# Kernel tuning notes

Hardware: AMD Instinct MI355X
Metric: run time of the kernel (lower is better)

## Reference

```python
import jax, jax.numpy as jnp
import numpy as np

B, T, N, D = 16, 24, 2048, 64
L, K = 2, 3  # num_layers, cheb_k


def setup_inputs() -> dict:
    key = jax.random.key(0)
    ks = jax.random.split(key, 6)
    x = jax.random.normal(ks[0], (B, T, N, D), dtype=jnp.float32)
    init_state = jnp.zeros((L, B, N, D), dtype=jnp.float32)
    adj = jax.random.uniform(ks[1], (N, N), dtype=jnp.float32)
    adj = adj / jnp.sum(adj, axis=-1, keepdims=True)  # row-normalized adjacency
    cin = 2 * D
    Wg = jax.random.normal(ks[2], (L, K, cin, 2 * D), dtype=jnp.float32) * (1.0 / np.sqrt(K * cin))
    bg = jnp.zeros((L, 2 * D), dtype=jnp.float32)
    Wu = jax.random.normal(ks[3], (L, K, cin, D), dtype=jnp.float32) * (1.0 / np.sqrt(K * cin))
    bu = jnp.zeros((L, D), dtype=jnp.float32)
    return {"x": x, "init_state": init_state, "adj_matrix": adj,
            "Wg": Wg, "bg": bg, "Wu": Wu, "bu": bu}


def _cheb_supports(adj, k):
    # T0=I, T1=A, Tk = 2*A@T_{k-1} - T_{k-2}
    n = adj.shape[0]
    sup = [jnp.eye(n, dtype=adj.dtype), adj]
    for _ in range(2, k):
        sup.append(2.0 * adj @ sup[-1] - sup[-2])
    return jnp.stack(sup[:k], axis=0)  # [K, N, N]


def _gconv(xs, supports, W, b):
    # xs: [B,N,Cin], supports: [K,N,N], W: [K,Cin,Cout]
    xg = jnp.einsum('knm,bmc->bknc', supports, xs)
    return jnp.einsum('bknc,kco->bno', xg, W) + b


def _cell(x_t, state, supports, Wg_l, bg_l, Wu_l, bu_l):
    ins = jnp.concatenate([x_t, state], axis=-1)  # [B,N,2D]
    zr = jax.nn.sigmoid(_gconv(ins, supports, Wg_l, bg_l))
    z, r = jnp.split(zr, 2, axis=-1)
    cand_in = jnp.concatenate([x_t, z * state], axis=-1)
    hc = jnp.tanh(_gconv(cand_in, supports, Wu_l, bu_l))
    return r * state + (1.0 - r) * hc


def reference(x, init_state, adj_matrix, Wg, bg, Wu, bu):
    supports = _cheb_supports(adj_matrix, K)
    current = x  # [B,T,N,D]
    hiddens = []
    for l in range(L):
        def step(state, x_t, l=l):
            new = _cell(x_t, state, supports, Wg[l], bg[l], Wu[l], bu[l])
            return new, new
        last, seq = jax.lax.scan(step, init_state[l], jnp.swapaxes(current, 0, 1))
        hiddens.append(last)
        current = x + jnp.swapaxes(seq, 0, 1)  # residual over the stacked states
    return current, jnp.stack(hiddens, axis=0)
```

## Files before the change

kernel.cpp:

```cpp
#include <hip/hip_runtime.h>
#include <hip/hip_bf16.h>
#include <math.h>

typedef __bf16 bf16x8 __attribute__((ext_vector_type(8)));
typedef float f32x4 __attribute__((ext_vector_type(4)));
typedef __hip_bfloat16 bf16s;

constexpr int kB = 16, kT = 24, kN = 2048, kD = 64;
constexpr size_t kBND = (size_t)kB * kN * kD;

struct SlotDesc { const void* p; int astr; int trow; int isF32; };
struct Slots6 { SlotDesc s[6]; };
struct DiffGrp { const bf16s* src; bf16s* oA; bf16s* oA2; };
struct DiffP { const bf16s* S0; const bf16s* S1; DiffGrp g[4]; int colsPerGrp; };

__device__ __forceinline__ void async_copy16(void* lds, const void* g) {
  __builtin_amdgcn_global_load_lds((const __attribute__((address_space(1))) void*)g,
                                   (__attribute__((address_space(3))) void*)lds,
                                   16, 0, 0);
}


__device__ __forceinline__ void diff_core(
    const bf16s* __restrict__ S, const bf16s* __restrict__ Bsrc,
    int m0, int c0, bf16s* lA, bf16s* lB, f32x4 (&acc)[4][4])
{
  const int tid = threadIdx.x, lane = tid & 63, wave = tid >> 6;
  const int wm = (wave >> 1) * 64, wn = (wave & 1) * 64;
  const f32x4 zero = {0.f, 0.f, 0.f, 0.f};
#pragma unroll
  for (int i = 0; i < 4; ++i)
#pragma unroll
    for (int j = 0; j < 4; ++j) acc[i][j] = zero;

  const int ra = tid >> 3;
  const int cs = ((tid & 7) ^ (ra & 7)) * 8;
  const int rk0 = (((lane >> 4)) ^ (lane & 7)) * 8;
  const int rk1 = ((4 + (lane >> 4)) ^ (lane & 7)) * 8;

  for (int k0 = 0; k0 < 2048; k0 += 64) {
#pragma unroll
    for (int i = 0; i < 4; ++i)
      async_copy16(lA + (size_t)(i * 256 + tid) * 8,
                   S + (size_t)(m0 + i * 32 + ra) * 2048 + k0 + cs);
#pragma unroll
    for (int i = 0; i < 4; ++i)
      async_copy16(lB + (size_t)(i * 256 + tid) * 8,
                   Bsrc + (size_t)(c0 + i * 32 + ra) * 2048 + k0 + cs);
    __syncthreads();
#pragma unroll
    for (int ks = 0; ks < 2; ++ks) {
      const int rk = ks ? rk1 : rk0;
      bf16x8 av[4], bv[4];
#pragma unroll
      for (int f = 0; f < 4; ++f) {
        av[f] = *(const bf16x8*)(lA + (size_t)(wm + f * 16 + (lane & 15)) * 64 + rk);
        bv[f] = *(const bf16x8*)(lB + (size_t)(wn + f * 16 + (lane & 15)) * 64 + rk);
      }
#pragma unroll
      for (int i = 0; i < 4; ++i)
#pragma unroll
        for (int j = 0; j < 4; ++j)
          acc[i][j] = __builtin_amdgcn_mfma_f32_16x16x32_bf16(av[i], bv[j], acc[i][j], 0, 0, 0);
    }
    __syncthreads();
  }
}

__global__ __launch_bounds__(256) void k_diff(DiffP p)
{
  __shared__ bf16s lA[128 * 64];
  __shared__ bf16s lB[128 * 64];
  const int mi = blockIdx.x;
  const bf16s* S = (mi >> 4) ? p.S1 : p.S0;
  const int m0 = (mi & 15) * 128;
  const int ybpg = p.colsPerGrp >> 7;
  const int grp = blockIdx.y / ybpg;
  const int c0 = (blockIdx.y - grp * ybpg) * 128;
  const DiffGrp G = p.g[grp];

  f32x4 acc[4][4];
  diff_core(S, G.src, m0, c0, lA, lB, acc);

  bf16s* out = (mi >> 4) ? G.oA2 : G.oA;
  const int lane = threadIdx.x & 63, wave = threadIdx.x >> 6;
  const int wm = (wave >> 1) * 64, wn = (wave & 1) * 64;
  const int rq = (lane >> 4) * 4, cl = lane & 15;
#pragma unroll
  for (int fm = 0; fm < 4; ++fm)
#pragma unroll
    for (int fn = 0; fn < 4; ++fn)
#pragma unroll
      for (int q = 0; q < 4; ++q) {
        int gm = m0 + wm + fm * 16 + rq + q;
        int gc = c0 + wn + fn * 16 + cl;
        size_t off = ((size_t)(gc >> 6) * 2048 + gm) * 64 + (gc & 63);
        out[off] = __float2bfloat16(acc[fm][fn][q]);
      }
}

__global__ __launch_bounds__(256) void k_a2(
    const bf16s* __restrict__ A, const bf16s* __restrict__ AT, bf16s* A2)
{
  __shared__ bf16s lA[128 * 64];
  __shared__ bf16s lB[128 * 64];
  const int m0 = blockIdx.x * 128, n0 = blockIdx.y * 128;
  f32x4 acc[4][4];
  diff_core(A, AT, m0, n0, lA, lB, acc);
  const int lane = threadIdx.x & 63, wave = threadIdx.x >> 6;
  const int wm = (wave >> 1) * 64, wn = (wave & 1) * 64;
  const int rq = (lane >> 4) * 4, cl = lane & 15;
#pragma unroll
  for (int fm = 0; fm < 4; ++fm)
#pragma unroll
    for (int fn = 0; fn < 4; ++fn)
#pragma unroll
      for (int q = 0; q < 4; ++q) {
        int gm = m0 + wm + fm * 16 + rq + q;
        int gc = n0 + wn + fn * 16 + cl;
        A2[(size_t)gm * 2048 + gc] = __float2bfloat16(2.f * acc[fm][fn][q] - (gm == gc ? 1.f : 0.f));
      }
}

template<int BN>
__device__ __forceinline__ void small_core(
    const Slots6& sl, int m0, const bf16s* __restrict__ W,
    bf16s* lA, bf16s* lB, f32x4 (&acc)[4][BN / 32])
{
  const int tid = threadIdx.x, lane = tid & 63, wave = tid >> 6;
  const int wm = (wave >> 1) * 64, wn = (wave & 1) * (BN / 2);
  const f32x4 zero = {0.f, 0.f, 0.f, 0.f};
#pragma unroll
  for (int i = 0; i < 4; ++i)
#pragma unroll
    for (int j = 0; j < BN / 32; ++j) acc[i][j] = zero;

  const int ra = tid >> 3;
  const int cs = ((tid & 7) ^ (ra & 7)) * 8;
  const int rk0 = (((lane >> 4)) ^ (lane & 7)) * 8;
  const int rk1 = ((4 + (lane >> 4)) ^ (lane & 7)) * 8;

#pragma unroll
  for (int ks = 0; ks < 6; ++ks) {
    const SlotDesc sd = sl.s[ks];
    if (!sd.isF32) {
      const bf16s* base = (const bf16s*)sd.p;
#pragma unroll
      for (int i = 0; i < 4; ++i) {
        int row = m0 + i * 32 + ra;
        size_t roff = ((size_t)(row >> 11) * sd.astr + sd.trow + (row & 2047)) * 64 + cs;
        async_copy16(lA + (size_t)(i * 256 + tid) * 8, base + roff);
      }
    } else {
#pragma unroll
      for (int i = 0; i < 4; ++i) {
        int row = m0 + i * 32 + ra;
        size_t roff = ((size_t)(row >> 11) * sd.astr + sd.trow + (row & 2047)) * 64 + cs;
        const float4* q0 = (const float4*)((const float*)sd.p + roff);
        float4 a = q0[0], b = q0[1];
        union { bf16x8 v; bf16s h[8]; } u;
        u.h[0] = __float2bfloat16(a.x); u.h[1] = __float2bfloat16(a.y);
        u.h[2] = __float2bfloat16(a.z); u.h[3] = __float2bfloat16(a.w);
        u.h[4] = __float2bfloat16(b.x); u.h[5] = __float2bfloat16(b.y);
        u.h[6] = __float2bfloat16(b.z); u.h[7] = __float2bfloat16(b.w);
        *(bf16x8*)(lA + (size_t)(i * 256 + tid) * 8) = u.v;
      }
    }
#pragma unroll
    for (int i = 0; i < BN / 32; ++i)
      async_copy16(lB + (size_t)(i * 256 + tid) * 8,
                   W + (size_t)(i * 32 + ra) * 384 + ks * 64 + cs);
    __syncthreads();
#pragma unroll
    for (int kss = 0; kss < 2; ++kss) {
      const int rk = kss ? rk1 : rk0;
      bf16x8 av[4], bv[BN / 32];
#pragma unroll
      for (int f = 0; f < 4; ++f)
        av[f] = *(const bf16x8*)(lA + (size_t)(wm + f * 16 + (lane & 15)) * 64 + rk);
#pragma unroll
      for (int f = 0; f < BN / 32; ++f)
        bv[f] = *(const bf16x8*)(lB + (size_t)(wn + f * 16 + (lane & 15)) * 64 + rk);
#pragma unroll
      for (int i = 0; i < 4; ++i)
#pragma unroll
        for (int j = 0; j < BN / 32; ++j)
          acc[i][j] = __builtin_amdgcn_mfma_f32_16x16x32_bf16(av[i], bv[j], acc[i][j], 0, 0, 0);
    }
    __syncthreads();
  }
}

struct LayerG {
  Slots6 sl; const bf16s* W; const float* bias;
  const float* h; bf16s* zh; bf16s* zhT; float* r;
};
__global__ __launch_bounds__(256) void k_gate(LayerG A, LayerG B, int nA)
{
  __shared__ bf16s lA[128 * 64];
  __shared__ bf16s lB[128 * 64];
  const int bx = blockIdx.x;
  const bool isA = bx < nA;
  const LayerG L = isA ? A : B;
  const int m0 = (isA ? bx : bx - nA) * 128;
  f32x4 acc[4][4];
  small_core<128>(L.sl, m0, L.W, lA, lB, acc);
  const int lane = threadIdx.x & 63, wave = threadIdx.x >> 6;
  const int wm = (wave >> 1) * 64, wn = (wave & 1) * 64;
  const int rq = (lane >> 4) * 4, cl = lane & 15;
#pragma unroll
  for (int fm = 0; fm < 4; ++fm)
#pragma unroll
    for (int fn = 0; fn < 4; ++fn) {
      const int o = wn + fn * 16 + cl;
      const float bias = L.bias[o];
#pragma unroll
      for (int q = 0; q < 4; ++q) {
        size_t gm = (size_t)m0 + wm + fm * 16 + rq + q;
        float s = 1.f / (1.f + expf(-(acc[fm][fn][q] + bias)));
        if (o < 64) {
          float zh = s * L.h[gm * 64 + o];
          L.zh[gm * 64 + o] = __float2bfloat16(zh);
          L.zhT[((size_t)((gm >> 11) * 64 + o)) * 2048 + (gm & 2047)] = __float2bfloat16(zh);
        } else {
          L.r[gm * 64 + (o - 64)] = s;
        }
      }
    }
}

struct LayerC {
  Slots6 sl; const bf16s* W; const float* bias;
  const float* r; float* h32; bf16s* hT; bf16s* h_bf; float* hid;
  bf16s* x1; bf16s* x1T;
  float* outC;
  const float* x0; int t;
};
__global__ __launch_bounds__(256) void k_cand(LayerC A, LayerC B, int nA)
{
  __shared__ bf16s lA[128 * 64];
  __shared__ bf16s lB[64 * 64];
  const int bx = blockIdx.x;
  const bool isA = bx < nA;
  const LayerC L = isA ? A : B;
  const int m0 = (isA ? bx : bx - nA) * 128;
  f32x4 acc[4][2];
  small_core<64>(L.sl, m0, L.W, lA, lB, acc);
  const int lane = threadIdx.x & 63, wave = threadIdx.x >> 6;
  const int wm = (wave >> 1) * 64, wn = (wave & 1) * 32;
  const int rq = (lane >> 4) * 4, cl = lane & 15;
#pragma unroll
  for (int fm = 0; fm < 4; ++fm)
#pragma unroll
    for (int fn = 0; fn < 2; ++fn) {
      const int d = wn + fn * 16 + cl;
      const float bias = L.bias[d];
#pragma unroll
      for (int q = 0; q < 4; ++q) {
        size_t gm = (size_t)m0 + wm + fm * 16 + rq + q;
        float hc = tanhf(acc[fm][fn][q] + bias);
        float r = L.r[gm * 64 + d];
        float h = L.h32[gm * 64 + d];
        float hn = r * h + (1.f - r) * hc;
        L.h32[gm * 64 + d] = hn;
        int b = (int)(gm >> 11), n = (int)(gm & 2047);
        L.hT[((size_t)(b * 64 + d)) * 2048 + n] = __float2bfloat16(hn);
        L.h_bf[gm * 64 + d] = __float2bfloat16(hn);
        size_t xi = (((size_t)b * kT + L.t) * 2048 + n) * 64 + d;
        if (L.x1) {
          float xv = L.x0[xi] + hn;
          L.x1[gm * 64 + d] = __float2bfloat16(xv);
          L.x1T[((size_t)(b * 64 + d)) * 2048 + n] = __float2bfloat16(xv);
        }
        if (L.outC) L.outC[xi] = L.x0[xi] + hn;
        if (L.hid) L.hid[gm * 64 + d] = hn;
      }
    }
}

__global__ __launch_bounds__(256) void transpose_cvt(
    const float* in, bf16s* out, int nrows, int ncols,
    size_t in_ostride, size_t out_ostride)
{
  __shared__ float tile[64][65];
  const int r0 = blockIdx.x * 64, c0 = blockIdx.y * 64;
  in  += (size_t)blockIdx.z * in_ostride;
  out += (size_t)blockIdx.z * out_ostride;
  const int tx = threadIdx.x & 63, ty = threadIdx.x >> 6;
#pragma unroll
  for (int i = 0; i < 64; i += 4)
    tile[ty + i][tx] = in[(size_t)(r0 + ty + i) * ncols + c0 + tx];
  __syncthreads();
#pragma unroll
  for (int i = 0; i < 64; i += 4)
    out[(size_t)(c0 + ty + i) * nrows + r0 + tx] = __float2bfloat16(tile[tx][ty + i]);
}

__global__ __launch_bounds__(256) void k_cvt(const float* in, bf16s* out, int n)
{
  int i = blockIdx.x * 256 + threadIdx.x;
  if (i < n) out[i] = __float2bfloat16(in[i]);
}

__global__ __launch_bounds__(256) void k_repack(
    const float* Wg, const float* Wu, bf16s* WgT, bf16s* WuT)
{
  int idx = blockIdx.x * 256 + threadIdx.x;
  if (idx < 2 * 3 * 128 * 128) {
    int o = idx & 127, cin = (idx >> 7) & 127, k = (idx >> 14) % 3, l = idx / 49152;
    WgT[((size_t)(l * 128 + o)) * 384 + (2 * k + (cin >> 6)) * 64 + (cin & 63)] =
        __float2bfloat16(Wg[idx]);
  }
  if (idx < 2 * 3 * 128 * 64) {
    int o = idx & 63, cin = (idx >> 6) & 127, k = (idx >> 13) % 3, l = idx / 24576;
    WuT[((size_t)(l * 64 + o)) * 384 + (2 * k + (cin >> 6)) * 64 + (cin & 63)] =
        __float2bfloat16(Wu[idx]);
  }
}

__global__ __launch_bounds__(256) void init_layer(
    const float* ist_l, float* h32, bf16s* hT, bf16s* h_bf)
{
  size_t idx = (size_t)blockIdx.x * 256 + threadIdx.x;
  if (idx >= kBND) return;
  int d = (int)(idx & 63);
  size_t row = idx >> 6;
  int n = (int)(row & 2047), b = (int)(row >> 11);
  float h = ist_l[idx];
  h32[idx] = h;
  hT[((size_t)(b * 64 + d)) * 2048 + n] = __float2bfloat16(h);
  h_bf[idx] = __float2bfloat16(h);
}

extern "C" void kernel_launch(void* const* d_in, const int* in_sizes, int n_in,
                              void* d_out, int out_size, void* d_ws, size_t ws_size,
                              hipStream_t stream)
{
  (void)in_sizes; (void)n_in; (void)out_size;
  const float* x   = (const float*)d_in[0];
  const float* ist = (const float*)d_in[1];
  const float* adj = (const float*)d_in[2];
  const float* Wg  = (const float*)d_in[3];
  const float* bg  = (const float*)d_in[4];
  const float* Wu  = (const float*)d_in[5];
  const float* bu  = (const float*)d_in[6];
  float* outCur = (float*)d_out;
  float* outHid = outCur + (size_t)kB * kT * kN * kD;

  char* p = (char*)d_ws;
  auto carve = [&](size_t bytes) { char* q = p; p += (bytes + 255) & ~(size_t)255; return q; };
  bf16s* A_bf  = (bf16s*)carve((size_t)2048 * 2048 * 2);
  bf16s* A2_bf = (bf16s*)carve((size_t)2048 * 2048 * 2);
  bf16s* WgT   = (bf16s*)carve((size_t)2 * 128 * 384 * 2);
  bf16s* WuT   = (bf16s*)carve((size_t)2 * 64 * 384 * 2);
  float* h32b  = (float*)carve(2 * kBND * 4);
  float* r32b  = (float*)carve(2 * kBND * 4);
  bf16s* hTb   = (bf16s*)carve(2 * kBND * 2);
  bf16s* hbfb  = (bf16s*)carve(2 * kBND * 2);
  bf16s* zhTb  = (bf16s*)carve(2 * kBND * 2);
  bf16s* zhbfb = (bf16s*)carve(2 * kBND * 2);
  bf16s* x1_bf = (bf16s*)carve(kBND * 2);
  bf16s* x1T   = (bf16s*)carve(kBND * 2);
  bf16s* sAh0  = (bf16s*)carve(kBND * 2);
  bf16s* sA2h0 = (bf16s*)carve(kBND * 2);
  bf16s* sAh1  = (bf16s*)carve(kBND * 2);
  bf16s* sA2h1 = (bf16s*)carve(kBND * 2);
  bf16s* sAx1  = (bf16s*)carve(kBND * 2);
  bf16s* sA2x1 = (bf16s*)carve(kBND * 2);

  float* h32_0 = h32b;            float* h32_1 = h32b + kBND;
  float* r32_0 = r32b;            float* r32_1 = r32b + kBND;
  bf16s* hT0 = hTb;               bf16s* hT1 = hTb + kBND;
  bf16s* hbf0 = hbfb;             bf16s* hbf1 = hbfb + kBND;
  bf16s* zhT0 = zhTb;             bf16s* zhT1 = zhTb + kBND;
  bf16s* zhbf0 = zhbfb;           bf16s* zhbf1 = zhbfb + kBND;

  size_t used = (size_t)(p - (char*)d_ws);
  size_t rem = (ws_size > used) ? ws_size - used : 0;
  const size_t xTfull = (size_t)kB * kT * kD * kN * 2;
  bool batched0 = rem >= (xTfull / 2 + 2 * xTfull + (1 << 20));

  bf16s *AT_bf, *AxF = nullptr, *A2xF = nullptr, *xTh = nullptr;
  bf16s *x0T = nullptr, *sAx0 = nullptr, *sA2x0 = nullptr;
  if (batched0) {
    AxF  = (bf16s*)carve(xTfull);
    A2xF = (bf16s*)carve(xTfull);
    xTh  = (bf16s*)carve(xTfull / 2);
    AT_bf = AxF;
  } else {
    AT_bf = (bf16s*)carve((size_t)2048 * 2048 * 2);
    x0T   = (bf16s*)carve(kBND * 2);
    sAx0  = (bf16s*)carve(kBND * 2);
    sA2x0 = (bf16s*)carve(kBND * 2);
  }

  k_cvt<<<dim3((2048 * 2048 + 255) / 256), 256, 0, stream>>>(adj, A_bf, 2048 * 2048);
  transpose_cvt<<<dim3(32, 32, 1), 256, 0, stream>>>(adj, AT_bf, 2048, 2048, 0, 0);
  k_a2<<<dim3(16, 16, 1), 256, 0, stream>>>(A_bf, AT_bf, A2_bf);
  k_repack<<<dim3(384), 256, 0, stream>>>(Wg, Wu, WgT, WuT);
  init_layer<<<dim3((int)(kBND / 256)), 256, 0, stream>>>(ist, h32_0, hT0, hbf0);
  init_layer<<<dim3((int)(kBND / 256)), 256, 0, stream>>>(ist + kBND, h32_1, hT1, hbf1);

  if (batched0) {
    for (int h = 0; h < 2; ++h) {
      size_t off = (size_t)h * 8 * kT * 131072;
      transpose_cvt<<<dim3(32, 1, 8 * kT), 256, 0, stream>>>(x + off, xTh, 2048, 64, 131072, 131072);
      DiffP dp; dp.S0 = A_bf; dp.S1 = A2_bf; dp.colsPerGrp = 12288;
      dp.g[0] = DiffGrp{xTh, AxF + off, A2xF + off};
      dp.g[1] = dp.g[2] = dp.g[3] = DiffGrp{nullptr, nullptr, nullptr};
      k_diff<<<dim3(32, 96), 256, 0, stream>>>(dp);
    }
  }

  for (int s = 0; s <= kT; ++s) {
    const bool aA = (s < kT), aB = (s >= 1);
    const int tA = s, tB = s - 1;
    const int nA = aA ? 256 : 0, nB = aB ? 256 : 0;

    if (aA && !batched0)
      transpose_cvt<<<dim3(32, 1, kB), 256, 0, stream>>>(
          x + (size_t)tA * 131072, x0T, 2048, 64, (size_t)kT * 131072, 131072);

    {
      DiffP dp; dp.S0 = A_bf; dp.S1 = A2_bf; dp.colsPerGrp = 1024;
      int ng = 0;
      if (aA)              dp.g[ng++] = DiffGrp{hT0, sAh0, sA2h0};
      if (aA && !batched0) dp.g[ng++] = DiffGrp{x0T, sAx0, sA2x0};
      if (aB) { dp.g[ng++] = DiffGrp{hT1, sAh1, sA2h1};
                dp.g[ng++] = DiffGrp{x1T, sAx1, sA2x1}; }
      for (int i = ng; i < 4; ++i) dp.g[i] = DiffGrp{nullptr, nullptr, nullptr};
      k_diff<<<dim3(32, 8 * ng), 256, 0, stream>>>(dp);
    }

    {
      LayerG GA = {}, GB = {};
      if (aA) {
        GA.sl.s[0] = SlotDesc{x, kT * 2048, tA * 2048, 1};
        GA.sl.s[1] = SlotDesc{hbf0, 2048, 0, 0};
        GA.sl.s[2] = batched0 ? SlotDesc{AxF,  kT * 2048, tA * 2048, 0} : SlotDesc{sAx0, 2048, 0, 0};
        GA.sl.s[3] = SlotDesc{sAh0, 2048, 0, 0};
        GA.sl.s[4] = batched0 ? SlotDesc{A2xF, kT * 2048, tA * 2048, 0} : SlotDesc{sA2x0, 2048, 0, 0};
        GA.sl.s[5] = SlotDesc{sA2h0, 2048, 0, 0};
        GA.W = WgT; GA.bias = bg; GA.h = h32_0; GA.zh = zhbf0; GA.zhT = zhT0; GA.r = r32_0;
      }
      if (aB) {
        GB.sl.s[0] = SlotDesc{x1_bf, 2048, 0, 0};
        GB.sl.s[1] = SlotDesc{hbf1, 2048, 0, 0};
        GB.sl.s[2] = SlotDesc{sAx1, 2048, 0, 0};
        GB.sl.s[3] = SlotDesc{sAh1, 2048, 0, 0};
        GB.sl.s[4] = SlotDesc{sA2x1, 2048, 0, 0};
        GB.sl.s[5] = SlotDesc{sA2h1, 2048, 0, 0};
        GB.W = WgT + (size_t)128 * 384; GB.bias = bg + 128;
        GB.h = h32_1; GB.zh = zhbf1; GB.zhT = zhT1; GB.r = r32_1;
      }
      k_gate<<<dim3(nA + nB), 256, 0, stream>>>(GA, GB, nA);
    }

    {
      DiffP dp; dp.S0 = A_bf; dp.S1 = A2_bf; dp.colsPerGrp = 1024;
      int ng = 0;
      if (aA) dp.g[ng++] = DiffGrp{zhT0, sAh0, sA2h0};
      if (aB) dp.g[ng++] = DiffGrp{zhT1, sAh1, sA2h1};
      for (int i = ng; i < 4; ++i) dp.g[i] = DiffGrp{nullptr, nullptr, nullptr};
      k_diff<<<dim3(32, 8 * ng), 256, 0, stream>>>(dp);
    }

    {
      LayerC CA = {}, CB = {};
      if (aA) {
        CA.sl = LayerG{}.sl;
        CA.sl.s[0] = SlotDesc{x, kT * 2048, tA * 2048, 1};
        CA.sl.s[1] = SlotDesc{zhbf0, 2048, 0, 0};
        CA.sl.s[2] = batched0 ? SlotDesc{AxF,  kT * 2048, tA * 2048, 0} : SlotDesc{sAx0, 2048, 0, 0};
        CA.sl.s[3] = SlotDesc{sAh0, 2048, 0, 0};
        CA.sl.s[4] = batched0 ? SlotDesc{A2xF, kT * 2048, tA * 2048, 0} : SlotDesc{sA2x0, 2048, 0, 0};
        CA.sl.s[5] = SlotDesc{sA2h0, 2048, 0, 0};
        CA.W = WuT; CA.bias = bu; CA.r = r32_0; CA.h32 = h32_0; CA.hT = hT0; CA.h_bf = hbf0;
        CA.hid = (tA == kT - 1) ? outHid : nullptr;
        CA.x1 = x1_bf; CA.x1T = x1T; CA.outC = nullptr; CA.x0 = x; CA.t = tA;
      }
      if (aB) {
        CB.sl.s[0] = SlotDesc{x1_bf, 2048, 0, 0};
        CB.sl.s[1] = SlotDesc{zhbf1, 2048, 0, 0};
        CB.sl.s[2] = SlotDesc{sAx1, 2048, 0, 0};
        CB.sl.s[3] = SlotDesc{sAh1, 2048, 0, 0};
        CB.sl.s[4] = SlotDesc{sA2x1, 2048, 0, 0};
        CB.sl.s[5] = SlotDesc{sA2h1, 2048, 0, 0};
        CB.W = WuT + (size_t)64 * 384; CB.bias = bu + 64;
        CB.r = r32_1; CB.h32 = h32_1; CB.hT = hT1; CB.h_bf = hbf1;
        CB.hid = (tB == kT - 1) ? outHid + kBND : nullptr;
        CB.x1 = nullptr; CB.x1T = nullptr; CB.outC = outCur; CB.x0 = x; CB.t = tB;
      }
      k_cand<<<dim3(nA + nB), 256, 0, stream>>>(CA, CB, nA);
    }
  }
}
```

Measured before the change: 5.224 ms.

## Exploit linearity to drop layer-1 x diffusion; fuse A and A2 diffusion per block

Layer 1's input is x + h0_new, so A·x1 is rebuilt as A·x + A·h0 from the already computed per-step diffusion of layer 0's state and the batched x diffusion. This removes the x1 transpose and its per-step diffusion GEMMs, and the candidate stage adds two bf16 operands while loading. A new 512-thread diffusion kernel computes A·B and A²·B in one block, sharing the B tile in LDS across both supports. The batched x path is now always used, and the candidate diffusion outputs go to separate buffers so that sAh0 is not overwritten. The sum is formed from bf16 values, which adds a small precision risk.

```diff
diff --git a/kernel.cpp b/kernel.cpp
--- a/kernel.cpp
+++ b/kernel.cpp
@@ -9,10 +9,9 @@
 constexpr int kB = 16, kT = 24, kN = 2048, kD = 64;
 constexpr size_t kBND = (size_t)kB * kN * kD;
 
-struct SlotDesc { const void* p; int astr; int trow; int isF32; };
-struct Slots6 { SlotDesc s[6]; };
-struct DiffGrp { const bf16s* src; bf16s* oA; bf16s* oA2; };
-struct DiffP { const bf16s* S0; const bf16s* S1; DiffGrp g[4]; int colsPerGrp; };
+struct Slot { const void* p0; const void* p1; int astr0, trow0, astr1, trow1, type; };
+struct Slots6 { Slot s[6]; };
+struct DiffSrc { const bf16s* src; bf16s* oA; bf16s* oA2; };
 
 __device__ __forceinline__ void async_copy16(void* lds, const void* g) {
   __builtin_amdgcn_global_load_lds((const __attribute__((address_space(1))) void*)g,
@@ -21,12 +20,24 @@
 }
 
 
-__device__ __forceinline__ void diff_core(
-    const bf16s* __restrict__ S, const bf16s* __restrict__ Bsrc,
-    int m0, int c0, bf16s* lA, bf16s* lB, f32x4 (&acc)[4][4])
-{
+__global__ __launch_bounds__(512) void k_diff4(
+    const bf16s* __restrict__ S0, const bf16s* __restrict__ S1,
+    DiffSrc g0, DiffSrc g1, int ctPerSrc)
+{
+  __shared__ bf16s lA0[128 * 64];
+  __shared__ bf16s lA1[128 * 64];
+  __shared__ bf16s lB[128 * 64];
+  const int m0 = blockIdx.x * 128;
+  const int grp = blockIdx.y / ctPerSrc;
+  const int c0 = (blockIdx.y - grp * ctPerSrc) * 128;
+  const DiffSrc G = grp ? g1 : g0;
+
   const int tid = threadIdx.x, lane = tid & 63, wave = tid >> 6;
-  const int wm = (wave >> 1) * 64, wn = (wave & 1) * 64;
+  const int sp = wave & 1, qd = wave >> 1;
+  const int wm = (qd >> 1) * 64, wn = (qd & 1) * 64;
+  const bf16s* lAsel = sp ? lA1 : lA0;
+
+  f32x4 acc[4][4];
   const f32x4 zero = {0.f, 0.f, 0.f, 0.f};
 #pragma unroll
   for (int i = 0; i < 4; ++i)
@@ -35,18 +46,22 @@
 
   const int ra = tid >> 3;
   const int cs = ((tid & 7) ^ (ra & 7)) * 8;
-  const int rk0 = (((lane >> 4)) ^ (lane & 7)) * 8;
+  const int rk0 = ((lane >> 4) ^ (lane & 7)) * 8;
   const int rk1 = ((4 + (lane >> 4)) ^ (lane & 7)) * 8;
 
   for (int k0 = 0; k0 < 2048; k0 += 64) {
 #pragma unroll
-    for (int i = 0; i < 4; ++i)
-      async_copy16(lA + (size_t)(i * 256 + tid) * 8,
-                   S + (size_t)(m0 + i * 32 + ra) * 2048 + k0 + cs);
-#pragma unroll
-    for (int i = 0; i < 4; ++i)
-      async_copy16(lB + (size_t)(i * 256 + tid) * 8,
-                   Bsrc + (size_t)(c0 + i * 32 + ra) * 2048 + k0 + cs);
+    for (int i = 0; i < 2; ++i)
+      async_copy16(lA0 + (size_t)(i * 512 + tid) * 8,
+                   S0 + (size_t)(m0 + i * 64 + ra) * 2048 + k0 + cs);
+#pragma unroll
+    for (int i = 0; i < 2; ++i)
+      async_copy16(lA1 + (size_t)(i * 512 + tid) * 8,
+                   S1 + (size_t)(m0 + i * 64 + ra) * 2048 + k0 + cs);
+#pragma unroll
+    for (int i = 0; i < 2; ++i)
+      async_copy16(lB + (size_t)(i * 512 + tid) * 8,
+                   G.src + (size_t)(c0 + i * 64 + ra) * 2048 + k0 + cs);
     __syncthreads();
 #pragma unroll
     for (int ks = 0; ks < 2; ++ks) {
@@ -54,7 +69,7 @@
       bf16x8 av[4], bv[4];
 #pragma unroll
       for (int f = 0; f < 4; ++f) {
-        av[f] = *(const bf16x8*)(lA + (size_t)(wm + f * 16 + (lane & 15)) * 64 + rk);
+        av[f] = *(const bf16x8*)(lAsel + (size_t)(wm + f * 16 + (lane & 15)) * 64 + rk);
         bv[f] = *(const bf16x8*)(lB + (size_t)(wn + f * 16 + (lane & 15)) * 64 + rk);
       }
 #pragma unroll
@@ -65,26 +80,8 @@
     }
     __syncthreads();
   }
-}
-
-__global__ __launch_bounds__(256) void k_diff(DiffP p)
-{
-  __shared__ bf16s lA[128 * 64];
-  __shared__ bf16s lB[128 * 64];
-  const int mi = blockIdx.x;
-  const bf16s* S = (mi >> 4) ? p.S1 : p.S0;
-  const int m0 = (mi & 15) * 128;
-  const int ybpg = p.colsPerGrp >> 7;
-  const int grp = blockIdx.y / ybpg;
-  const int c0 = (blockIdx.y - grp * ybpg) * 128;
-  const DiffGrp G = p.g[grp];
-
-  f32x4 acc[4][4];
-  diff_core(S, G.src, m0, c0, lA, lB, acc);
-
-  bf16s* out = (mi >> 4) ? G.oA2 : G.oA;
-  const int lane = threadIdx.x & 63, wave = threadIdx.x >> 6;
-  const int wm = (wave >> 1) * 64, wn = (wave & 1) * 64;
+
+  bf16s* out = sp ? G.oA2 : G.oA;
   const int rq = (lane >> 4) * 4, cl = lane & 15;
 #pragma unroll
   for (int fm = 0; fm < 4; ++fm)
@@ -97,6 +94,49 @@
         size_t off = ((size_t)(gc >> 6) * 2048 + gm) * 64 + (gc & 63);
         out[off] = __float2bfloat16(acc[fm][fn][q]);
       }
+}
+
+__device__ __forceinline__ void diff_core(
+    const bf16s* __restrict__ S, const bf16s* __restrict__ Bsrc,
+    int m0, int c0, bf16s* lA, bf16s* lB, f32x4 (&acc)[4][4])
+{
+  const int tid = threadIdx.x, lane = tid & 63, wave = tid >> 6;
+  const int wm = (wave >> 1) * 64, wn = (wave & 1) * 64;
+  const f32x4 zero = {0.f, 0.f, 0.f, 0.f};
+#pragma unroll
+  for (int i = 0; i < 4; ++i)
+#pragma unroll
+    for (int j = 0; j < 4; ++j) acc[i][j] = zero;
+  const int ra = tid >> 3;
+  const int cs = ((tid & 7) ^ (ra & 7)) * 8;
+  const int rk0 = ((lane >> 4) ^ (lane & 7)) * 8;
+  const int rk1 = ((4 + (lane >> 4)) ^ (lane & 7)) * 8;
+  for (int k0 = 0; k0 < 2048; k0 += 64) {
+#pragma unroll
+    for (int i = 0; i < 4; ++i) {
+      async_copy16(lA + (size_t)(i * 256 + tid) * 8,
+                   S + (size_t)(m0 + i * 32 + ra) * 2048 + k0 + cs);
+      async_copy16(lB + (size_t)(i * 256 + tid) * 8,
+                   Bsrc + (size_t)(c0 + i * 32 + ra) * 2048 + k0 + cs);
+    }
+    __syncthreads();
+#pragma unroll
+    for (int ks = 0; ks < 2; ++ks) {
+      const int rk = ks ? rk1 : rk0;
+      bf16x8 av[4], bv[4];
+#pragma unroll
+      for (int f = 0; f < 4; ++f) {
+        av[f] = *(const bf16x8*)(lA + (size_t)(wm + f * 16 + (lane & 15)) * 64 + rk);
+        bv[f] = *(const bf16x8*)(lB + (size_t)(wn + f * 16 + (lane & 15)) * 64 + rk);
+      }
+#pragma unroll
+      for (int i = 0; i < 4; ++i)
+#pragma unroll
+        for (int j = 0; j < 4; ++j)
+          acc[i][j] = __builtin_amdgcn_mfma_f32_16x16x32_bf16(av[i], bv[j], acc[i][j], 0, 0, 0);
+    }
+    __syncthreads();
+  }
 }
 
 __global__ __launch_bounds__(256) void k_a2(
@@ -137,26 +177,26 @@
 
   const int ra = tid >> 3;
   const int cs = ((tid & 7) ^ (ra & 7)) * 8;
-  const int rk0 = (((lane >> 4)) ^ (lane & 7)) * 8;
+  const int rk0 = ((lane >> 4) ^ (lane & 7)) * 8;
   const int rk1 = ((4 + (lane >> 4)) ^ (lane & 7)) * 8;
 
 #pragma unroll
   for (int ks = 0; ks < 6; ++ks) {
-    const SlotDesc sd = sl.s[ks];
-    if (!sd.isF32) {
-      const bf16s* base = (const bf16s*)sd.p;
+    const Slot sd = sl.s[ks];
+    if (sd.type == 0) {
+      const bf16s* base = (const bf16s*)sd.p0;
 #pragma unroll
       for (int i = 0; i < 4; ++i) {
         int row = m0 + i * 32 + ra;
-        size_t roff = ((size_t)(row >> 11) * sd.astr + sd.trow + (row & 2047)) * 64 + cs;
+        size_t roff = ((size_t)(row >> 11) * sd.astr0 + sd.trow0 + (row & 2047)) * 64 + cs;
         async_copy16(lA + (size_t)(i * 256 + tid) * 8, base + roff);
       }
-    } else {
+    } else if (sd.type == 1) {
 #pragma unroll
       for (int i = 0; i < 4; ++i) {
         int row = m0 + i * 32 + ra;
-        size_t roff = ((size_t)(row >> 11) * sd.astr + sd.trow + (row & 2047)) * 64 + cs;
-        const float4* q0 = (const float4*)((const float*)sd.p + roff);
+        size_t roff = ((size_t)(row >> 11) * sd.astr0 + sd.trow0 + (row & 2047)) * 64 + cs;
+        const float4* q0 = (const float4*)((const float*)sd.p0 + roff);
         float4 a = q0[0], b = q0[1];
         union { bf16x8 v; bf16s h[8]; } u;
         u.h[0] = __float2bfloat16(a.x); u.h[1] = __float2bfloat16(a.y);
@@ -164,6 +204,20 @@
         u.h[4] = __float2bfloat16(b.x); u.h[5] = __float2bfloat16(b.y);
         u.h[6] = __float2bfloat16(b.z); u.h[7] = __float2bfloat16(b.w);
         *(bf16x8*)(lA + (size_t)(i * 256 + tid) * 8) = u.v;
+      }
+    } else {
+#pragma unroll
+      for (int i = 0; i < 4; ++i) {
+        int row = m0 + i * 32 + ra;
+        size_t r0o = ((size_t)(row >> 11) * sd.astr0 + sd.trow0 + (row & 2047)) * 64 + cs;
+        size_t r1o = ((size_t)(row >> 11) * sd.astr1 + sd.trow1 + (row & 2047)) * 64 + cs;
+        union { bf16x8 v; bf16s h[8]; } a, b, o;
+        a.v = *(const bf16x8*)((const bf16s*)sd.p0 + r0o);
+        b.v = *(const bf16x8*)((const bf16s*)sd.p1 + r1o);
+#pragma unroll
+        for (int j = 0; j < 8; ++j)
+          o.h[j] = __float2bfloat16(__bfloat162float(a.h[j]) + __bfloat162float(b.h[j]));
+        *(bf16x8*)(lA + (size_t)(i * 256 + tid) * 8) = o.v;
       }
     }
 #pragma unroll
@@ -232,7 +286,7 @@
 struct LayerC {
   Slots6 sl; const bf16s* W; const float* bias;
   const float* r; float* h32; bf16s* hT; bf16s* h_bf; float* hid;
-  bf16s* x1; bf16s* x1T;
+  bf16s* x1;
   float* outC;
   const float* x0; int t;
 };
@@ -267,11 +321,7 @@
         L.hT[((size_t)(b * 64 + d)) * 2048 + n] = __float2bfloat16(hn);
         L.h_bf[gm * 64 + d] = __float2bfloat16(hn);
         size_t xi = (((size_t)b * kT + L.t) * 2048 + n) * 64 + d;
-        if (L.x1) {
-          float xv = L.x0[xi] + hn;
-          L.x1[gm * 64 + d] = __float2bfloat16(xv);
-          L.x1T[((size_t)(b * 64 + d)) * 2048 + n] = __float2bfloat16(xv);
-        }
+        if (L.x1) L.x1[gm * 64 + d] = __float2bfloat16(L.x0[xi] + hn);
         if (L.outC) L.outC[xi] = L.x0[xi] + hn;
         if (L.hid) L.hid[gm * 64 + d] = hn;
       }
@@ -336,7 +386,7 @@
                               void* d_out, int out_size, void* d_ws, size_t ws_size,
                               hipStream_t stream)
 {
-  (void)in_sizes; (void)n_in; (void)out_size;
+  (void)in_sizes; (void)n_in; (void)out_size; (void)ws_size;
   const float* x   = (const float*)d_in[0];
   const float* ist = (const float*)d_in[1];
   const float* adj = (const float*)d_in[2];
@@ -359,40 +409,27 @@
   bf16s* hbfb  = (bf16s*)carve(2 * kBND * 2);
   bf16s* zhTb  = (bf16s*)carve(2 * kBND * 2);
   bf16s* zhbfb = (bf16s*)carve(2 * kBND * 2);
-  bf16s* x1_bf = (bf16s*)carve(kBND * 2);
-  bf16s* x1T   = (bf16s*)carve(kBND * 2);
+  bf16s* x1b   = (bf16s*)carve(2 * kBND * 2);
   bf16s* sAh0  = (bf16s*)carve(kBND * 2);
   bf16s* sA2h0 = (bf16s*)carve(kBND * 2);
   bf16s* sAh1  = (bf16s*)carve(kBND * 2);
   bf16s* sA2h1 = (bf16s*)carve(kBND * 2);
-  bf16s* sAx1  = (bf16s*)carve(kBND * 2);
-  bf16s* sA2x1 = (bf16s*)carve(kBND * 2);
-
-  float* h32_0 = h32b;            float* h32_1 = h32b + kBND;
-  float* r32_0 = r32b;            float* r32_1 = r32b + kBND;
-  bf16s* hT0 = hTb;               bf16s* hT1 = hTb + kBND;
-  bf16s* hbf0 = hbfb;             bf16s* hbf1 = hbfb + kBND;
-  bf16s* zhT0 = zhTb;             bf16s* zhT1 = zhTb + kBND;
-  bf16s* zhbf0 = zhbfb;           bf16s* zhbf1 = zhbfb + kBND;
-
-  size_t used = (size_t)(p - (char*)d_ws);
-  size_t rem = (ws_size > used) ? ws_size - used : 0;
+  bf16s* sZ0   = (bf16s*)carve(kBND * 2);
+  bf16s* sA2Z0 = (bf16s*)carve(kBND * 2);
+  bf16s* sZ1   = (bf16s*)carve(kBND * 2);
+  bf16s* sA2Z1 = (bf16s*)carve(kBND * 2);
   const size_t xTfull = (size_t)kB * kT * kD * kN * 2;
-  bool batched0 = rem >= (xTfull / 2 + 2 * xTfull + (1 << 20));
-
-  bf16s *AT_bf, *AxF = nullptr, *A2xF = nullptr, *xTh = nullptr;
-  bf16s *x0T = nullptr, *sAx0 = nullptr, *sA2x0 = nullptr;
-  if (batched0) {
-    AxF  = (bf16s*)carve(xTfull);
-    A2xF = (bf16s*)carve(xTfull);
-    xTh  = (bf16s*)carve(xTfull / 2);
-    AT_bf = AxF;
-  } else {
-    AT_bf = (bf16s*)carve((size_t)2048 * 2048 * 2);
-    x0T   = (bf16s*)carve(kBND * 2);
-    sAx0  = (bf16s*)carve(kBND * 2);
-    sA2x0 = (bf16s*)carve(kBND * 2);
-  }
+  bf16s* AxF  = (bf16s*)carve(xTfull);
+  bf16s* A2xF = (bf16s*)carve(xTfull);
+  bf16s* xTh  = (bf16s*)carve(xTfull / 2);
+  bf16s* AT_bf = AxF;
+
+  float* h32_0 = h32b;   float* h32_1 = h32b + kBND;
+  float* r32_0 = r32b;   float* r32_1 = r32b + kBND;
+  bf16s* hT0 = hTb;      bf16s* hT1 = hTb + kBND;
+  bf16s* hbf0 = hbfb;    bf16s* hbf1 = hbfb + kBND;
+  bf16s* zhT0 = zhTb;    bf16s* zhT1 = zhTb + kBND;
+  bf16s* zhbf0 = zhbfb;  bf16s* zhbf1 = zhbfb + kBND;
 
   k_cvt<<<dim3((2048 * 2048 + 255) / 256), 256, 0, stream>>>(adj, A_bf, 2048 * 2048);
   transpose_cvt<<<dim3(32, 32, 1), 256, 0, stream>>>(adj, AT_bf, 2048, 2048, 0, 0);
@@ -401,55 +438,51 @@
   init_layer<<<dim3((int)(kBND / 256)), 256, 0, stream>>>(ist, h32_0, hT0, hbf0);
   init_layer<<<dim3((int)(kBND / 256)), 256, 0, stream>>>(ist + kBND, h32_1, hT1, hbf1);
 
-  if (batched0) {
-    for (int h = 0; h < 2; ++h) {
-      size_t off = (size_t)h * 8 * kT * 131072;
-      transpose_cvt<<<dim3(32, 1, 8 * kT), 256, 0, stream>>>(x + off, xTh, 2048, 64, 131072, 131072);
-      DiffP dp; dp.S0 = A_bf; dp.S1 = A2_bf; dp.colsPerGrp = 12288;
-      dp.g[0] = DiffGrp{xTh, AxF + off, A2xF + off};
-      dp.g[1] = dp.g[2] = dp.g[3] = DiffGrp{nullptr, nullptr, nullptr};
-      k_diff<<<dim3(32, 96), 256, 0, stream>>>(dp);
-    }
-  }
+  for (int h = 0; h < 2; ++h) {
+    size_t off = (size_t)h * 8 * kT * 131072;
+    transpose_cvt<<<dim3(32, 1, 8 * kT), 256, 0, stream>>>(x + off, xTh, 2048, 64, 131072, 131072);
+    k_diff4<<<dim3(16, 96), 512, 0, stream>>>(
+        A_bf, A2_bf, DiffSrc{xTh, AxF + off, A2xF + off}, DiffSrc{}, 96);
+  }
+
+  auto Sb = [](const void* p0, int astr, int trow) {
+    return Slot{p0, nullptr, astr, trow, 0, 0, 0};
+  };
+  auto Sf = [](const void* p0, int astr, int trow) {
+    return Slot{p0, nullptr, astr, trow, 0, 0, 1};
+  };
+  auto S2 = [](const void* p0, const void* p1, int astr1, int trow1) {
+    return Slot{p0, p1, 2048, 0, astr1, trow1, 2};
+  };
 
   for (int s = 0; s <= kT; ++s) {
     const bool aA = (s < kT), aB = (s >= 1);
     const int tA = s, tB = s - 1;
     const int nA = aA ? 256 : 0, nB = aB ? 256 : 0;
-
-    if (aA && !batched0)
-      transpose_cvt<<<dim3(32, 1, kB), 256, 0, stream>>>(
-          x + (size_t)tA * 131072, x0T, 2048, 64, (size_t)kT * 131072, 131072);
-
-    {
-      DiffP dp; dp.S0 = A_bf; dp.S1 = A2_bf; dp.colsPerGrp = 1024;
-      int ng = 0;
-      if (aA)              dp.g[ng++] = DiffGrp{hT0, sAh0, sA2h0};
-      if (aA && !batched0) dp.g[ng++] = DiffGrp{x0T, sAx0, sA2x0};
-      if (aB) { dp.g[ng++] = DiffGrp{hT1, sAh1, sA2h1};
-                dp.g[ng++] = DiffGrp{x1T, sAx1, sA2x1}; }
-      for (int i = ng; i < 4; ++i) dp.g[i] = DiffGrp{nullptr, nullptr, nullptr};
-      k_diff<<<dim3(32, 8 * ng), 256, 0, stream>>>(dp);
-    }
+    bf16s* x1cur = x1b + (size_t)(s & 1) * kBND;
+    bf16s* x1prev = x1b + (size_t)((s - 1) & 1) * kBND;
+
+    k_diff4<<<dim3(16, aB ? 16 : 8), 512, 0, stream>>>(
+        A_bf, A2_bf, DiffSrc{hT0, sAh0, sA2h0}, DiffSrc{hT1, sAh1, sA2h1}, 8);
 
     {
       LayerG GA = {}, GB = {};
       if (aA) {
-        GA.sl.s[0] = SlotDesc{x, kT * 2048, tA * 2048, 1};
-        GA.sl.s[1] = SlotDesc{hbf0, 2048, 0, 0};
-        GA.sl.s[2] = batched0 ? SlotDesc{AxF,  kT * 2048, tA * 2048, 0} : SlotDesc{sAx0, 2048, 0, 0};
-        GA.sl.s[3] = SlotDesc{sAh0, 2048, 0, 0};
-        GA.sl.s[4] = batched0 ? SlotDesc{A2xF, kT * 2048, tA * 2048, 0} : SlotDesc{sA2x0, 2048, 0, 0};
-        GA.sl.s[5] = SlotDesc{sA2h0, 2048, 0, 0};
+        GA.sl.s[0] = Sf(x, kT * 2048, tA * 2048);
+        GA.sl.s[1] = Sb(hbf0, 2048, 0);
+        GA.sl.s[2] = Sb(AxF, kT * 2048, tA * 2048);
+        GA.sl.s[3] = Sb(sAh0, 2048, 0);
+        GA.sl.s[4] = Sb(A2xF, kT * 2048, tA * 2048);
+        GA.sl.s[5] = Sb(sA2h0, 2048, 0);
         GA.W = WgT; GA.bias = bg; GA.h = h32_0; GA.zh = zhbf0; GA.zhT = zhT0; GA.r = r32_0;
       }
       if (aB) {
-        GB.sl.s[0] = SlotDesc{x1_bf, 2048, 0, 0};
-        GB.sl.s[1] = SlotDesc{hbf1, 2048, 0, 0};
-        GB.sl.s[2] = SlotDesc{sAx1, 2048, 0, 0};
-        GB.sl.s[3] = SlotDesc{sAh1, 2048, 0, 0};
-        GB.sl.s[4] = SlotDesc{sA2x1, 2048, 0, 0};
-        GB.sl.s[5] = SlotDesc{sA2h1, 2048, 0, 0};
+        GB.sl.s[0] = Sb(x1prev, 2048, 0);
+        GB.sl.s[1] = Sb(hbf1, 2048, 0);
+        GB.sl.s[2] = S2(sAh0, AxF, kT * 2048, tB * 2048);
+        GB.sl.s[3] = Sb(sAh1, 2048, 0);
+        GB.sl.s[4] = S2(sA2h0, A2xF, kT * 2048, tB * 2048);
+        GB.sl.s[5] = Sb(sA2h1, 2048, 0);
         GB.W = WgT + (size_t)128 * 384; GB.bias = bg + 128;
         GB.h = h32_1; GB.zh = zhbf1; GB.zhT = zhT1; GB.r = r32_1;
       }
@@ -457,39 +490,39 @@
     }
 
     {
-      DiffP dp; dp.S0 = A_bf; dp.S1 = A2_bf; dp.colsPerGrp = 1024;
-      int ng = 0;
-      if (aA) dp.g[ng++] = DiffGrp{zhT0, sAh0, sA2h0};
-      if (aB) dp.g[ng++] = DiffGrp{zhT1, sAh1, sA2h1};
-      for (int i = ng; i < 4; ++i) dp.g[i] = DiffGrp{nullptr, nullptr, nullptr};
-      k_diff<<<dim3(32, 8 * ng), 256, 0, stream>>>(dp);
+      DiffSrc d0{zhT0, sZ0, sA2Z0}, d1{zhT1, sZ1, sA2Z1};
+      if (aA && aB)
+        k_diff4<<<dim3(16, 16), 512, 0, stream>>>(A_bf, A2_bf, d0, d1, 8);
+      else if (aA)
+        k_diff4<<<dim3(16, 8), 512, 0, stream>>>(A_bf, A2_bf, d0, d1, 8);
+      else
+        k_diff4<<<dim3(16, 8), 512, 0, stream>>>(A_bf, A2_bf, d1, d0, 8);
     }
 
     {
       LayerC CA = {}, CB = {};
       if (aA) {
-        CA.sl = LayerG{}.sl;
-        CA.sl.s[0] = SlotDesc{x, kT * 2048, tA * 2048, 1};
-        CA.sl.s[1] = SlotDesc{zhbf0, 2048, 0, 0};
-        CA.sl.s[2] = batched0 ? SlotDesc{AxF,  kT * 2048, tA * 2048, 0} : SlotDesc{sAx0, 2048, 0, 0};
-        CA.sl.s[3] = SlotDesc{sAh0, 2048, 0, 0};
-        CA.sl.s[4] = batched0 ? SlotDesc{A2xF, kT * 2048, tA * 2048, 0} : SlotDesc{sA2x0, 2048, 0, 0};
-        CA.sl.s[5] = SlotDesc{sA2h0, 2048, 0, 0};
+        CA.sl.s[0] = Sf(x, kT * 2048, tA * 2048);
+        CA.sl.s[1] = Sb(zhbf0, 2048, 0);
+        CA.sl.s[2] = Sb(AxF, kT * 2048, tA * 2048);
+        CA.sl.s[3] = Sb(sZ0, 2048, 0);
+        CA.sl.s[4] = Sb(A2xF, kT * 2048, tA * 2048);
+        CA.sl.s[5] = Sb(sA2Z0, 2048, 0);
         CA.W = WuT; CA.bias = bu; CA.r = r32_0; CA.h32 = h32_0; CA.hT = hT0; CA.h_bf = hbf0;
         CA.hid = (tA == kT - 1) ? outHid : nullptr;
-        CA.x1 = x1_bf; CA.x1T = x1T; CA.outC = nullptr; CA.x0 = x; CA.t = tA;
+        CA.x1 = x1cur; CA.outC = nullptr; CA.x0 = x; CA.t = tA;
       }
       if (aB) {
-        CB.sl.s[0] = SlotDesc{x1_bf, 2048, 0, 0};
-        CB.sl.s[1] = SlotDesc{zhbf1, 2048, 0, 0};
-        CB.sl.s[2] = SlotDesc{sAx1, 2048, 0, 0};
-        CB.sl.s[3] = SlotDesc{sAh1, 2048, 0, 0};
-        CB.sl.s[4] = SlotDesc{sA2x1, 2048, 0, 0};
-        CB.sl.s[5] = SlotDesc{sA2h1, 2048, 0, 0};
+        CB.sl.s[0] = Sb(x1prev, 2048, 0);
+        CB.sl.s[1] = Sb(zhbf1, 2048, 0);
+        CB.sl.s[2] = S2(sAh0, AxF, kT * 2048, tB * 2048);
+        CB.sl.s[3] = Sb(sZ1, 2048, 0);
+        CB.sl.s[4] = S2(sA2h0, A2xF, kT * 2048, tB * 2048);
+        CB.sl.s[5] = Sb(sA2Z1, 2048, 0);
         CB.W = WuT + (size_t)64 * 384; CB.bias = bu + 64;
         CB.r = r32_1; CB.h32 = h32_1; CB.hT = hT1; CB.h_bf = hbf1;
         CB.hid = (tB == kT - 1) ? outHid + kBND : nullptr;
-        CB.x1 = nullptr; CB.x1T = nullptr; CB.outC = outCur; CB.x0 = x; CB.t = tB;
+        CB.x1 = nullptr; CB.outC = outCur; CB.x0 = x; CB.t = tB;
       }
       k_cand<<<dim3(nA + nB), 256, 0, stream>>>(CA, CB, nA);
     }
```

Result: slower. 5.509 ms (+5.4%).
